# Kernel optimization log

Measured on AMD Instinct MI355X. Metric: run time of the kernel, lower is better.

Reference implementation:

```python
import jax, jax.numpy as jnp
import numpy as np

D_IN = 1024
D_OUT = 1024
NUM_HEADS = 16
HEAD_DIM = D_OUT // NUM_HEADS


def setup_inputs() -> dict:
    key = jax.random.key(0)
    kx, kq, kk, kv, ko = jax.random.split(key, 5)
    s = 1.0 / np.sqrt(D_IN)
    return {
        "x": jax.random.normal(kx, (1, 4096, D_IN), dtype=jnp.float32),
        "Wq": jax.random.normal(kq, (D_IN, D_OUT), dtype=jnp.float32) * s,
        "Wk": jax.random.normal(kk, (D_IN, D_OUT), dtype=jnp.float32) * s,
        "Wv": jax.random.normal(kv, (D_IN, D_OUT), dtype=jnp.float32) * s,
        "Wo": jax.random.normal(ko, (D_OUT, D_OUT), dtype=jnp.float32) * s,
    }


def reference(x, Wq, Wk, Wv, Wo):
    b, s, _ = x.shape
    # project and split heads: [b, h, s, d]
    def split_heads(t):
        return t.reshape(b, s, NUM_HEADS, HEAD_DIM).transpose(0, 2, 1, 3)
    Q = split_heads(x @ Wq)
    K = split_heads(x @ Wk)
    V = split_heads(x @ Wv)
    scores = jnp.einsum("bhqd,bhkd->bhqk", Q, K) / jnp.sqrt(jnp.float32(HEAD_DIM))
    causal = jnp.triu(jnp.ones((s, s), dtype=bool), k=1)  # True above diagonal
    scores = jnp.where(causal, -jnp.inf, scores)
    probs = jax.nn.softmax(scores, axis=-1)
    out = jnp.einsum("bhqk,bhkd->bhqd", probs, V)
    out = out.transpose(0, 2, 1, 3).reshape(b, s, D_OUT)
    return out @ Wo
```

## Files before the change

kernel.cpp:

```cpp
#include <hip/hip_runtime.h>
#include <cstdint>

#define S_LEN 4096
#define D_MODEL 1024
#define NHEAD 16
#define HDIM 64

typedef __bf16 bf16_t;
typedef __bf16 bf16x8 __attribute__((ext_vector_type(8)));
typedef __bf16 bf16x4 __attribute__((ext_vector_type(4)));
typedef float floatx4 __attribute__((ext_vector_type(4)));

#define QSCALE 0.18033688011112042f

__device__ __forceinline__ void lds_cp16(void* lds, const void* g) {
    __builtin_amdgcn_global_load_lds(
        (const __attribute__((address_space(1))) unsigned int*)g,
        (__attribute__((address_space(3))) unsigned int*)lds,
        16, 0, 0);
}

__device__ __forceinline__ float fast_exp2(float x) {
    float r;
    asm("v_exp_f32 %0, %1" : "=v"(r) : "v"(x));
    return r;
}

__global__ __launch_bounds__(256) void k_prep(const float* __restrict__ x,
                                              const float* __restrict__ Wq,
                                              const float* __restrict__ Wk,
                                              const float* __restrict__ Wv,
                                              const float* __restrict__ Wo,
                                              bf16_t* __restrict__ xb,
                                              bf16_t* __restrict__ WtQKV,
                                              bf16_t* __restrict__ WtO) {
    const int bx = blockIdx.x;
    if (bx < 4096) {
        int i = bx * 256 + threadIdx.x;
        float4 v = ((const float4*)x)[i];
        bf16x4 o;
        o[0] = (bf16_t)v.x; o[1] = (bf16_t)v.y; o[2] = (bf16_t)v.z; o[3] = (bf16_t)v.w;
        *(bf16x4*)(xb + (size_t)i * 4) = o;
        return;
    }
    __shared__ float lds[64][65];
    const int i = bx - 4096;
    const int z = i >> 8, rem = i & 255;
    const float* W = (z == 0) ? Wq : (z == 1) ? Wk : (z == 2) ? Wv : Wo;
    bf16_t* Wt = (z < 3) ? (WtQKV + (size_t)z * 1048576) : WtO;
    const int k0 = (rem >> 4) * 64, n0 = (rem & 15) * 64;
    const int t = threadIdx.x, cl = t & 63, rl = t >> 6;
#pragma unroll
    for (int r = 0; r < 16; ++r)
        lds[r * 4 + rl][cl] = W[(size_t)(k0 + r * 4 + rl) * 1024 + n0 + cl];
    __syncthreads();
#pragma unroll
    for (int r = 0; r < 16; ++r)
        Wt[(size_t)(n0 + r * 4 + rl) * 1024 + k0 + cl] = (bf16_t)lds[cl][r * 4 + rl];
}

template <int MODE, int MT>
__global__ __launch_bounds__(256) void k_gemm(const bf16_t* __restrict__ A,
                                              const bf16_t* __restrict__ Bt,
                                              float* __restrict__ Cout,
                                              bf16_t* __restrict__ Qb,
                                              bf16_t* __restrict__ Kb,
                                              bf16_t* __restrict__ Vt,
                                              const bf16_t* __restrict__ OP1x,
                                              const float* __restrict__ Lpx) {
    constexpr int MI = MT / 32;
    __shared__ __align__(16) bf16_t sA[MT * 32];
    __shared__ __align__(16) bf16_t sB[128 * 32];
    const int t = threadIdx.x, w = t >> 6, lane = t & 63, quad = lane >> 4, l15 = lane & 15;
    const int m0 = blockIdx.x * MT, n0 = blockIdx.y * 128;
    const int wm = w >> 1, wn = w & 1;

    floatx4 acc[MI][4];
#pragma unroll
    for (int i = 0; i < MI; ++i)
#pragma unroll
        for (int j = 0; j < 4; ++j)
            acc[i][j] = floatx4{0.f, 0.f, 0.f, 0.f};

    const int crow = m0 + (t >> 2), ckq = t & 3;
    bf16x8 cA{}, cB{};
    float cla = 0.f, clb = 0.f;
    if (MODE == 2) {
        cA = *(const bf16x8*)(A + (size_t)crow * 1024 + ckq * 8);
        cB = *(const bf16x8*)(OP1x + (size_t)crow * 1024 + ckq * 8);
        cla = Lpx[crow];
        clb = Lpx[65536 + crow];
    }

    for (int kb = 0; kb < 32; ++kb) {
        __syncthreads();
        if (MODE == 2) {
            float inv = __builtin_amdgcn_rcpf(cla + clb);
            bf16x8 o;
#pragma unroll
            for (int e = 0; e < 8; ++e)
                o[e] = (bf16_t)(((float)cA[e] + (float)cB[e]) * inv);
            *(bf16x8*)&sA[t * 8] = o;
            if (kb + 1 < 32) {
                int h2 = (kb + 1) >> 1;
                int col = (kb + 1) * 32 + ckq * 8;
                cA = *(const bf16x8*)(A + (size_t)crow * 1024 + col);
                cB = *(const bf16x8*)(OP1x + (size_t)crow * 1024 + col);
                cla = Lpx[h2 * 4096 + crow];
                clb = Lpx[65536 + h2 * 4096 + crow];
            }
        } else {
#pragma unroll
            for (int r = 0; r < MT / 64; ++r) {
                int c = t + 256 * r;
                int row = c >> 2, kq = c & 3;
                lds_cp16(&sA[w * 512 + r * 2048],
                         A + (size_t)(m0 + row) * 1024 + kb * 32 + kq * 8);
            }
        }
#pragma unroll
        for (int r = 0; r < 2; ++r) {
            int c = t + 256 * r;
            int row = c >> 2, kq = c & 3;
            lds_cp16(&sB[w * 512 + r * 2048],
                     Bt + (size_t)(n0 + row) * 1024 + kb * 32 + kq * 8);
        }
        __syncthreads();
        bf16x8 af[MI], bfr[4];
#pragma unroll
        for (int i = 0; i < MI; ++i)
            af[i] = *(const bf16x8*)&sA[(wm * (MT / 2) + i * 16 + l15) * 32 + quad * 8];
#pragma unroll
        for (int j = 0; j < 4; ++j)
            bfr[j] = *(const bf16x8*)&sB[(wn * 64 + j * 16 + l15) * 32 + quad * 8];
#pragma unroll
        for (int i = 0; i < MI; ++i)
#pragma unroll
            for (int j = 0; j < 4; ++j)
                acc[i][j] = __builtin_amdgcn_mfma_f32_16x16x32_bf16(af[i], bfr[j],
                                                                    acc[i][j], 0, 0, 0);
    }

    const int mrow = m0 + wm * (MT / 2) + quad * 4;
    if (MODE == 0 || MODE == 2) {
        const int ncol = n0 + wn * 64 + l15;
#pragma unroll
        for (int i = 0; i < MI; ++i)
#pragma unroll
            for (int j = 0; j < 4; ++j)
#pragma unroll
                for (int r = 0; r < 4; ++r)
                    Cout[(size_t)(mrow + i * 16 + r) * 1024 + ncol + j * 16] = acc[i][j][r];
    } else {
        const int g = (int)blockIdx.y >> 3;
        const int ncbase = ((int)blockIdx.y & 7) * 128 + wn * 64 + l15;
        if (g == 2) {
#pragma unroll
            for (int j = 0; j < 4; ++j) {
                int nc = ncbase + j * 16;
                int hh = nc >> 6, dd = nc & 63;
                bf16_t* dst = Vt + (size_t)hh * 262144 + (size_t)dd * 64;
#pragma unroll
                for (int i = 0; i < MI; ++i) {
                    int s0r = mrow + i * 16;
                    bf16x4 pk;
                    pk[0] = (bf16_t)acc[i][j][0]; pk[1] = (bf16_t)acc[i][j][1];
                    pk[2] = (bf16_t)acc[i][j][2]; pk[3] = (bf16_t)acc[i][j][3];
                    int kk = s0r & 63;
                    int pp = (kk & 0x20) | ((kk & 0xC) << 1) | ((kk & 0x10) >> 2);
                    *(bf16x4*)&dst[(size_t)(s0r >> 6) * 4096 + pp] = pk;
                }
            }
        } else {
            bf16_t* base = g ? Kb : Qb;
            const float sc = g ? 1.0f : QSCALE;
#pragma unroll
            for (int j = 0; j < 4; ++j) {
                int nc = ncbase + j * 16;
                int hh = nc >> 6, dd = nc & 63;
#pragma unroll
                for (int i = 0; i < MI; ++i)
#pragma unroll
                    for (int r = 0; r < 4; ++r)
                        base[(size_t)hh * 262144 + (size_t)(mrow + i * 16 + r) * 64 + dd] =
                            (bf16_t)(acc[i][j][r] * sc);
            }
        }
    }
}

__global__ __launch_bounds__(128, 2) void k_attn(const bf16_t* __restrict__ Qb,
                                                 const bf16_t* __restrict__ Kb,
                                                 const bf16_t* __restrict__ Vt,
                                                 bf16_t* __restrict__ OP0,
                                                 bf16_t* __restrict__ OP1,
                                                 float* __restrict__ Lp) {
    __shared__ __align__(16) bf16_t Ks[2][64 * 64];
    __shared__ __align__(16) bf16_t Vts[2][64 * 64];
    const int bid = blockIdx.x;
    const int slot = bid >> 8, jj = bid & 255, g = jj >> 5, u = jj & 31;
    const int h = u >> 1, sp = u & 1;
    const int qb = (slot == 0) ? (31 - g) : (slot == 1) ? (16 + g)
                 : (slot == 2) ? (15 - g) : g;
    const int t = threadIdx.x, w = t >> 6, quad = (t & 63) >> 4, l15 = t & 15;
    const bf16_t* Qh = Qb + (size_t)h * 262144;
    const bf16_t* Kh = Kb + (size_t)h * 262144;
    const bf16_t* Vth = Vt + (size_t)h * 262144;

    const bf16_t* Qrow = Qh + (size_t)(qb * 128 + w * 64 + l15) * 64;
    bf16x8 bq[4][2];
#pragma unroll
    for (int qt = 0; qt < 4; ++qt)
#pragma unroll
        for (int kh = 0; kh < 2; ++kh)
            bq[qt][kh] = *(const bf16x8*)(Qrow + qt * 1024 + kh * 32 + quad * 8);

    float l_s[4] = {0.f, 0.f, 0.f, 0.f};
    floatx4 o_acc[4][4];
#pragma unroll
    for (int qt = 0; qt < 4; ++qt)
#pragma unroll
        for (int j = 0; j < 4; ++j) o_acc[qt][j] = floatx4{0.f, 0.f, 0.f, 0.f};

#define STAGE_K(b, kb_)                                                            \
    {                                                                              \
        _Pragma("unroll") for (int r = 0; r < 4; ++r) {                            \
            int c = t + 128 * r;                                                   \
            int row = c >> 3, sw = (c & 7) ^ (row & 7);                            \
            lds_cp16(&Ks[b][c * 8], Kh + (size_t)(kb_) * 4096 + row * 64 + sw * 8);\
        }                                                                          \
    }
#define STAGE_V(b, kb_)                                                            \
    {                                                                              \
        _Pragma("unroll") for (int r = 0; r < 4; ++r) {                            \
            int c = t + 128 * r;                                                   \
            int row = c >> 3, sw = (c & 7) ^ (row & 7);                            \
            lds_cp16(&Vts[b][c * 8], Vth + (size_t)(kb_) * 4096 + row * 64 + sw * 8);\
        }                                                                          \
    }

    const int t0 = sp ? (qb + 1) : 0;
    const int nIter = qb + 1;
    const int qmax = qb * 128 + w * 64 + 63;

    STAGE_K(0, t0)
    STAGE_V(0, t0)
    for (int it = 0; it < nIter; ++it) {
        const int kb = t0 + it;
        const int buf = it & 1;
        __syncthreads();
        if (it + 1 < nIter) {
            STAGE_K(buf ^ 1, kb + 1)
            STAGE_V(buf ^ 1, kb + 1)
        }
        const bool active = (kb * 64 <= qmax);

        if (active) {
            bf16x8 ak[4][2];
#pragma unroll
            for (int j = 0; j < 4; ++j) {
                int rk = j * 16 + l15;
                ak[j][0] = *(const bf16x8*)&Ks[buf][rk * 64 + ((quad ^ (rk & 7)) * 8)];
                ak[j][1] = *(const bf16x8*)&Ks[buf][rk * 64 + (((quad + 4) ^ (rk & 7)) * 8)];
            }
            floatx4 st[4][4];
            __builtin_amdgcn_s_setprio(1);
#pragma unroll
            for (int j = 0; j < 4; ++j)
#pragma unroll
                for (int qt = 0; qt < 4; ++qt) {
                    floatx4 z = {0.f, 0.f, 0.f, 0.f};
                    st[qt][j] = __builtin_amdgcn_mfma_f32_16x16x32_bf16(ak[j][0], bq[qt][0], z, 0, 0, 0);
                    st[qt][j] = __builtin_amdgcn_mfma_f32_16x16x32_bf16(ak[j][1], bq[qt][1], st[qt][j], 0, 0, 0);
                }
            __builtin_amdgcn_s_setprio(0);
            if (kb >= 2 * qb) {
#pragma unroll
                for (int qt = 0; qt < 4; ++qt) {
                    int qg = qb * 128 + w * 64 + qt * 16 + l15;
#pragma unroll
                    for (int j = 0; j < 4; ++j)
#pragma unroll
                        for (int r = 0; r < 4; ++r) {
                            int keyg = kb * 64 + j * 16 + quad * 4 + r;
                            if (keyg > qg) st[qt][j][r] = -1e30f;
                        }
                }
            }
            bf16x8 pa[4][2];
#pragma unroll
            for (int qt = 0; qt < 4; ++qt) {
                float a0 = 0.f, a1 = 0.f, a2 = 0.f, a3 = 0.f;
#pragma unroll
                for (int j = 0; j < 4; ++j) {
                    st[qt][j][0] = fast_exp2(st[qt][j][0]); a0 += st[qt][j][0];
                    st[qt][j][1] = fast_exp2(st[qt][j][1]); a1 += st[qt][j][1];
                    st[qt][j][2] = fast_exp2(st[qt][j][2]); a2 += st[qt][j][2];
                    st[qt][j][3] = fast_exp2(st[qt][j][3]); a3 += st[qt][j][3];
                }
                l_s[qt] += (a0 + a1) + (a2 + a3);
#pragma unroll
                for (int kh = 0; kh < 2; ++kh)
#pragma unroll
                    for (int m = 0; m < 4; ++m) {
                        pa[qt][kh][m]     = (bf16_t)st[qt][2 * kh][m];
                        pa[qt][kh][4 + m] = (bf16_t)st[qt][2 * kh + 1][m];
                    }
            }
            __builtin_amdgcn_s_setprio(1);
#pragma unroll
            for (int kh = 0; kh < 2; ++kh) {
                int pc = kh * 4 + quad;
#pragma unroll
                for (int j = 0; j < 4; ++j) {
                    int rd = j * 16 + l15;
                    bf16x8 bv = *(const bf16x8*)&Vts[buf][rd * 64 + ((pc ^ (rd & 7)) * 8)];
#pragma unroll
                    for (int qt = 0; qt < 4; ++qt)
                        o_acc[qt][j] = __builtin_amdgcn_mfma_f32_16x16x32_bf16(pa[qt][kh], bv, o_acc[qt][j], 0, 0, 0);
                }
            }
            __builtin_amdgcn_s_setprio(0);
        }
    }
    bf16_t* OPx = sp ? OP1 : OP0;
#pragma unroll
    for (int qt = 0; qt < 4; ++qt) {
        float l = l_s[qt];
        l += __shfl_xor(l, 16);
        l += __shfl_xor(l, 32);
        if (quad == 0)
            Lp[sp * 65536 + h * 4096 + (qb * 128 + w * 64 + qt * 16 + l15)] = l;
#pragma unroll
        for (int r = 0; r < 4; ++r) {
            int rowg = qb * 128 + w * 64 + qt * 16 + quad * 4 + r;
#pragma unroll
            for (int j = 0; j < 4; ++j)
                OPx[(size_t)rowg * 1024 + h * 64 + j * 16 + l15] = (bf16_t)o_acc[qt][j][r];
        }
    }
#undef STAGE_K
#undef STAGE_V
}

extern "C" void kernel_launch(void* const* d_in, const int* in_sizes, int n_in,
                              void* d_out, int out_size, void* d_ws, size_t ws_size,
                              hipStream_t stream) {
    const float* x  = (const float*)d_in[0];
    const float* Wq = (const float*)d_in[1];
    const float* Wk = (const float*)d_in[2];
    const float* Wv = (const float*)d_in[3];
    const float* Wo = (const float*)d_in[4];

    bf16_t* ws = (bf16_t*)d_ws;
    bf16_t* Xb    = ws;
    bf16_t* WtQKV = Xb + 4194304;
    bf16_t* WtO   = WtQKV + 3145728;
    bf16_t* Qb    = WtO + 1048576;
    bf16_t* Kb    = Qb + 4194304;
    bf16_t* Vt    = Kb + 4194304;
    bf16_t* OP1   = Vt + 4194304;
    bf16_t* OP0   = Xb;
    float*  Lp    = (float*)WtQKV;
    float* out = (float*)d_out;

    k_prep<<<5120, 256, 0, stream>>>(x, Wq, Wk, Wv, Wo, Xb, WtQKV, WtO);
    k_gemm<1, 128><<<dim3(32, 24), 256, 0, stream>>>(Xb, WtQKV, nullptr, Qb, Kb, Vt,
                                                     nullptr, nullptr);
    k_attn<<<1024, 128, 0, stream>>>(Qb, Kb, Vt, OP0, OP1, Lp);
    k_gemm<2, 64><<<dim3(64, 8), 256, 0, stream>>>(OP0, WtO, out, nullptr, nullptr,
                                                   nullptr, OP1, Lp);
}
```

Before: 199.7 us.

## Split attention across four waves, compute row sums via MFMA, swizzle GEMM blocks

The attention kernel now runs 256 threads per block, so each wave owns 32 query rows instead of 64. This halves per-wave register state and allows higher occupancy (launch bounds 256,4). The softmax row sums are now accumulated by an MFMA against a vector of ones rather than VALU adds plus shuffles. The GEMM kernels remap block indices in an XCD-aware way to improve L2 locality. The costs are more waves contending for the same K/V LDS tiles, extra MFMAs for the sums, and sums now taken from bf16-rounded probabilities.

```diff
diff --git a/kernel.cpp b/kernel.cpp
--- a/kernel.cpp
+++ b/kernel.cpp
@@ -69,10 +69,16 @@
                                               const bf16_t* __restrict__ OP1x,
                                               const float* __restrict__ Lpx) {
     constexpr int MI = MT / 32;
+    constexpr int GX = 4096 / MT;
+    constexpr int GY = (MODE == 1) ? 24 : 8;
+    constexpr int NWG = GX * GY;
     __shared__ __align__(16) bf16_t sA[MT * 32];
     __shared__ __align__(16) bf16_t sB[128 * 32];
     const int t = threadIdx.x, w = t >> 6, lane = t & 63, quad = lane >> 4, l15 = lane & 15;
-    const int m0 = blockIdx.x * MT, n0 = blockIdx.y * 128;
+    int lin = (int)blockIdx.y * GX + (int)blockIdx.x;
+    lin = (lin & 7) * (NWG / 8) + (lin >> 3);
+    const int bxr = lin % GX, byr = lin / GX;
+    const int m0 = bxr * MT, n0 = byr * 128;
     const int wm = w >> 1, wn = w & 1;
 
     floatx4 acc[MI][4];
@@ -152,8 +158,8 @@
                 for (int r = 0; r < 4; ++r)
                     Cout[(size_t)(mrow + i * 16 + r) * 1024 + ncol + j * 16] = acc[i][j][r];
     } else {
-        const int g = (int)blockIdx.y >> 3;
-        const int ncbase = ((int)blockIdx.y & 7) * 128 + wn * 64 + l15;
+        const int g = byr >> 3;
+        const int ncbase = (byr & 7) * 128 + wn * 64 + l15;
         if (g == 2) {
 #pragma unroll
             for (int j = 0; j < 4; ++j) {
@@ -189,7 +195,7 @@
     }
 }
 
-__global__ __launch_bounds__(128, 2) void k_attn(const bf16_t* __restrict__ Qb,
+__global__ __launch_bounds__(256, 4) void k_attn(const bf16_t* __restrict__ Qb,
                                                  const bf16_t* __restrict__ Kb,
                                                  const bf16_t* __restrict__ Vt,
                                                  bf16_t* __restrict__ OP0,
@@ -207,33 +213,39 @@
     const bf16_t* Kh = Kb + (size_t)h * 262144;
     const bf16_t* Vth = Vt + (size_t)h * 262144;
 
-    const bf16_t* Qrow = Qh + (size_t)(qb * 128 + w * 64 + l15) * 64;
-    bf16x8 bq[4][2];
-#pragma unroll
-    for (int qt = 0; qt < 4; ++qt)
+    const bf16_t* Qrow = Qh + (size_t)(qb * 128 + w * 32 + l15) * 64;
+    bf16x8 bq[2][2];
+#pragma unroll
+    for (int qt = 0; qt < 2; ++qt)
 #pragma unroll
         for (int kh = 0; kh < 2; ++kh)
             bq[qt][kh] = *(const bf16x8*)(Qrow + qt * 1024 + kh * 32 + quad * 8);
 
-    float l_s[4] = {0.f, 0.f, 0.f, 0.f};
-    floatx4 o_acc[4][4];
-#pragma unroll
-    for (int qt = 0; qt < 4; ++qt)
+    bf16x8 vones;
+#pragma unroll
+    for (int e = 0; e < 8; ++e) vones[e] = (bf16_t)1.0f;
+
+    floatx4 lacc[2];
+    floatx4 o_acc[2][4];
+#pragma unroll
+    for (int qt = 0; qt < 2; ++qt) {
+        lacc[qt] = floatx4{0.f, 0.f, 0.f, 0.f};
 #pragma unroll
         for (int j = 0; j < 4; ++j) o_acc[qt][j] = floatx4{0.f, 0.f, 0.f, 0.f};
+    }
 
 #define STAGE_K(b, kb_)                                                            \
     {                                                                              \
-        _Pragma("unroll") for (int r = 0; r < 4; ++r) {                            \
-            int c = t + 128 * r;                                                   \
+        _Pragma("unroll") for (int r = 0; r < 2; ++r) {                            \
+            int c = t + 256 * r;                                                   \
             int row = c >> 3, sw = (c & 7) ^ (row & 7);                            \
             lds_cp16(&Ks[b][c * 8], Kh + (size_t)(kb_) * 4096 + row * 64 + sw * 8);\
         }                                                                          \
     }
 #define STAGE_V(b, kb_)                                                            \
     {                                                                              \
-        _Pragma("unroll") for (int r = 0; r < 4; ++r) {                            \
-            int c = t + 128 * r;                                                   \
+        _Pragma("unroll") for (int r = 0; r < 2; ++r) {                            \
+            int c = t + 256 * r;                                                   \
             int row = c >> 3, sw = (c & 7) ^ (row & 7);                            \
             lds_cp16(&Vts[b][c * 8], Vth + (size_t)(kb_) * 4096 + row * 64 + sw * 8);\
         }                                                                          \
@@ -241,7 +253,7 @@
 
     const int t0 = sp ? (qb + 1) : 0;
     const int nIter = qb + 1;
-    const int qmax = qb * 128 + w * 64 + 63;
+    const int qmax = qb * 128 + w * 32 + 31;
 
     STAGE_K(0, t0)
     STAGE_V(0, t0)
@@ -256,28 +268,25 @@
         const bool active = (kb * 64 <= qmax);
 
         if (active) {
-            bf16x8 ak[4][2];
+            floatx4 st[2][4];
+            __builtin_amdgcn_s_setprio(1);
 #pragma unroll
             for (int j = 0; j < 4; ++j) {
                 int rk = j * 16 + l15;
-                ak[j][0] = *(const bf16x8*)&Ks[buf][rk * 64 + ((quad ^ (rk & 7)) * 8)];
-                ak[j][1] = *(const bf16x8*)&Ks[buf][rk * 64 + (((quad + 4) ^ (rk & 7)) * 8)];
-            }
-            floatx4 st[4][4];
-            __builtin_amdgcn_s_setprio(1);
-#pragma unroll
-            for (int j = 0; j < 4; ++j)
-#pragma unroll
-                for (int qt = 0; qt < 4; ++qt) {
+                bf16x8 a0 = *(const bf16x8*)&Ks[buf][rk * 64 + ((quad ^ (rk & 7)) * 8)];
+                bf16x8 a1 = *(const bf16x8*)&Ks[buf][rk * 64 + (((quad + 4) ^ (rk & 7)) * 8)];
+#pragma unroll
+                for (int qt = 0; qt < 2; ++qt) {
                     floatx4 z = {0.f, 0.f, 0.f, 0.f};
-                    st[qt][j] = __builtin_amdgcn_mfma_f32_16x16x32_bf16(ak[j][0], bq[qt][0], z, 0, 0, 0);
-                    st[qt][j] = __builtin_amdgcn_mfma_f32_16x16x32_bf16(ak[j][1], bq[qt][1], st[qt][j], 0, 0, 0);
-                }
+                    st[qt][j] = __builtin_amdgcn_mfma_f32_16x16x32_bf16(a0, bq[qt][0], z, 0, 0, 0);
+                    st[qt][j] = __builtin_amdgcn_mfma_f32_16x16x32_bf16(a1, bq[qt][1], st[qt][j], 0, 0, 0);
+                }
+            }
             __builtin_amdgcn_s_setprio(0);
             if (kb >= 2 * qb) {
 #pragma unroll
-                for (int qt = 0; qt < 4; ++qt) {
-                    int qg = qb * 128 + w * 64 + qt * 16 + l15;
+                for (int qt = 0; qt < 2; ++qt) {
+                    int qg = qb * 128 + w * 32 + qt * 16 + l15;
 #pragma unroll
                     for (int j = 0; j < 4; ++j)
 #pragma unroll
@@ -287,18 +296,16 @@
                         }
                 }
             }
-            bf16x8 pa[4][2];
-#pragma unroll
-            for (int qt = 0; qt < 4; ++qt) {
-                float a0 = 0.f, a1 = 0.f, a2 = 0.f, a3 = 0.f;
+            bf16x8 pa[2][2];
+#pragma unroll
+            for (int qt = 0; qt < 2; ++qt) {
 #pragma unroll
                 for (int j = 0; j < 4; ++j) {
-                    st[qt][j][0] = fast_exp2(st[qt][j][0]); a0 += st[qt][j][0];
-                    st[qt][j][1] = fast_exp2(st[qt][j][1]); a1 += st[qt][j][1];
-                    st[qt][j][2] = fast_exp2(st[qt][j][2]); a2 += st[qt][j][2];
-                    st[qt][j][3] = fast_exp2(st[qt][j][3]); a3 += st[qt][j][3];
-                }
-                l_s[qt] += (a0 + a1) + (a2 + a3);
+                    st[qt][j][0] = fast_exp2(st[qt][j][0]);
+                    st[qt][j][1] = fast_exp2(st[qt][j][1]);
+                    st[qt][j][2] = fast_exp2(st[qt][j][2]);
+                    st[qt][j][3] = fast_exp2(st[qt][j][3]);
+                }
 #pragma unroll
                 for (int kh = 0; kh < 2; ++kh)
 #pragma unroll
@@ -315,25 +322,24 @@
                 for (int j = 0; j < 4; ++j) {
                     int rd = j * 16 + l15;
                     bf16x8 bv = *(const bf16x8*)&Vts[buf][rd * 64 + ((pc ^ (rd & 7)) * 8)];
-#pragma unroll
-                    for (int qt = 0; qt < 4; ++qt)
-                        o_acc[qt][j] = __builtin_amdgcn_mfma_f32_16x16x32_bf16(pa[qt][kh], bv, o_acc[qt][j], 0, 0, 0);
-                }
+                    o_acc[0][j] = __builtin_amdgcn_mfma_f32_16x16x32_bf16(pa[0][kh], bv, o_acc[0][j], 0, 0, 0);
+                    o_acc[1][j] = __builtin_amdgcn_mfma_f32_16x16x32_bf16(pa[1][kh], bv, o_acc[1][j], 0, 0, 0);
+                }
+                lacc[0] = __builtin_amdgcn_mfma_f32_16x16x32_bf16(pa[0][kh], vones, lacc[0], 0, 0, 0);
+                lacc[1] = __builtin_amdgcn_mfma_f32_16x16x32_bf16(pa[1][kh], vones, lacc[1], 0, 0, 0);
             }
             __builtin_amdgcn_s_setprio(0);
         }
     }
     bf16_t* OPx = sp ? OP1 : OP0;
 #pragma unroll
-    for (int qt = 0; qt < 4; ++qt) {
-        float l = l_s[qt];
-        l += __shfl_xor(l, 16);
-        l += __shfl_xor(l, 32);
-        if (quad == 0)
-            Lp[sp * 65536 + h * 4096 + (qb * 128 + w * 64 + qt * 16 + l15)] = l;
+    for (int qt = 0; qt < 2; ++qt) {
+        if (l15 == 0)
+            *(floatx4*)&Lp[sp * 65536 + h * 4096 + qb * 128 + w * 32 + qt * 16 + quad * 4] =
+                lacc[qt];
 #pragma unroll
         for (int r = 0; r < 4; ++r) {
-            int rowg = qb * 128 + w * 64 + qt * 16 + quad * 4 + r;
+            int rowg = qb * 128 + w * 32 + qt * 16 + quad * 4 + r;
 #pragma unroll
             for (int j = 0; j < 4; ++j)
                 OPx[(size_t)rowg * 1024 + h * 64 + j * 16 + l15] = (bf16_t)o_acc[qt][j][r];
@@ -367,7 +373,7 @@
     k_prep<<<5120, 256, 0, stream>>>(x, Wq, Wk, Wv, Wo, Xb, WtQKV, WtO);
     k_gemm<1, 128><<<dim3(32, 24), 256, 0, stream>>>(Xb, WtQKV, nullptr, Qb, Kb, Vt,
                                                      nullptr, nullptr);
-    k_attn<<<1024, 128, 0, stream>>>(Qb, Kb, Vt, OP0, OP1, Lp);
+    k_attn<<<1024, 256, 0, stream>>>(Qb, Kb, Vt, OP0, OP1, Lp);
     k_gemm<2, 64><<<dim3(64, 8), 256, 0, stream>>>(OP0, WtO, out, nullptr, nullptr,
                                                    nullptr, OP1, Lp);
 }
```

Result: faster. 192.8 us (-3.5%).
